# Optimization experiments

Measured on AMD Instinct MI355X. Metric: run time of the kernel, lower is better.

## Reference

```python
import jax, jax.numpy as jnp
import numpy as np
from math import pi

B, CIN, COUT, H, W, K, STRIDE, PAD = 4, 32, 64, 32, 32, 3, 1, 1


def setup_inputs() -> dict:
    key = jax.random.key(0)
    k1, k2, k3 = jax.random.split(key, 3)
    x = jax.random.normal(k1, (B, CIN, H, W), dtype=jnp.float32)
    probe = jax.random.uniform(k2, (1, CIN, COUT, 1, 1, K, K), dtype=jnp.float32, minval=-pi, maxval=pi)
    out_w = jax.random.uniform(k3, (1, CIN, COUT, 1, 1, K, K), dtype=jnp.float32, minval=-pi, maxval=pi)
    return {"x": x, "probe": probe, "out_w": out_w}


def _patches(x):
    # sliding-window gather, equivalent to x.unfold(2,K,S).unfold(3,K,S)
    p = jax.lax.conv_general_dilated_patches(
        x, filter_shape=(K, K), window_strides=(STRIDE, STRIDE),
        padding=[(PAD, PAD), (PAD, PAD)])  # (B, CIN*K*K, Ho, Wo), channel-major
    b, _, ho, wo = p.shape
    p = p.reshape(b, CIN, K, K, ho, wo)
    return jnp.transpose(p, (0, 1, 4, 5, 2, 3))  # (B, CIN, Ho, Wo, K, K)


def reference(x, probe, out_w):
    pat = _patches(x)[:, :, None]                 # (B, CIN, 1, Ho, Wo, K, K)
    act = jnp.cos(pat - probe) ** 3               # (B, CIN, COUT, Ho, Wo, K, K)
    cw = jnp.cos(out_w).reshape(CIN, COUT, K, K)  # squeeze broadcast dims
    sw = jnp.sin(out_w).reshape(CIN, COUT, K, K)
    out_x = jnp.einsum('cokl,bcohwkl->bohw', cw, act)
    out_y = jnp.einsum('cokl,bcohwkl->bohw', sw, act)
    return jnp.arctan2(out_y, out_x)              # (B, COUT, Ho, Wo)
```

## Files before the change

### kernel.cpp

```cpp
#include <hip/hip_runtime.h>
#include <math.h>


typedef _Float16 half8 __attribute__((ext_vector_type(8)));
typedef _Float16 half4 __attribute__((ext_vector_type(4)));
typedef float floatx4 __attribute__((ext_vector_type(4)));

#define B_TAP_STRIDE (16 * 128 * 16)
#define B_VSTRIDE (9u * 16 * 128 * 16)

#define AL_OFF 26112

__global__ __launch_bounds__(256) void ring_prep_b(
    const float* __restrict__ probe, const float* __restrict__ outw,
    char* __restrict__ Bg) {
  int i = blockIdx.x * 256 + threadIdx.x;
  int q = i & 15;
  int n = (i >> 4) & 127;
  int tap = i >> 11;
  int o = n & 63;
  int xy = n >> 6;
  half8 hi, lo;
#pragma unroll
  for (int hf = 0; hf < 2; ++hf) {
    int c = q * 2 + hf;
    int idx = (c * 64 + o) * 9 + tap;
    float th = probe[idx];
    float wvv = outw[idx];
    float sth, cth, sw, cw;
    __sincosf(th, &sth, &cth);
    __sincosf(wvv, &sw, &cw);
    float c3 = cth * fmaf(4.0f * cth, cth, -3.0f);
    float s3 = sth * fmaf(-4.0f * sth, sth, 3.0f);
    float m = xy ? sw : cw;
    float v4[4] = {0.75f * m * cth, 0.75f * m * sth, 0.25f * m * c3,
                   0.25f * m * s3};
#pragma unroll
    for (int f = 0; f < 4; ++f) {
      _Float16 hv = (_Float16)v4[f];
      hi[hf * 4 + f] = hv;
      lo[hf * 4 + f] = (_Float16)((v4[f] - (float)hv) * 2048.0f);
    }
  }
  size_t off = (((size_t)tap * 16 + q) * 128 + n) * 16;
  *(half8*)(Bg + off) = hi;
  *(half8*)(Bg + off + B_VSTRIDE) = lo;
}

#define BLOAD2(dst, base)                    \
  do {                                       \
    dst##0 = *(const half8*)((base));        \
    dst##1 = *(const half8*)((base) + 8192); \
  } while (0)

__global__ __launch_bounds__(512, 2) void ring_mfma(
    const float* __restrict__ x, const char* __restrict__ Bg,
    float* __restrict__ out) {
  __shared__ __align__(16) char sA[52224];
  __shared__ __align__(16) float sR[4096];

  int blk = blockIdx.x;
  int oh = blk & 1;
  int h = (blk >> 1) & 31;
  int b = blk >> 6;
  int tid = threadIdx.x;

  int lane = tid & 63;
  int wv = tid >> 6;
  int n16 = lane & 15;
  int quad = lane >> 4;
  int kg = wv >> 2;
  int xy = (wv >> 1) & 1;
  int og = wv & 1;

  int n_global = xy * 64 + oh * 32 + og * 16 + n16;
  const char* bLane = Bg + (kg * 8 + quad) * 2048 + (size_t)n_global * 16;

  half8 BcH0, BcH1, BcL0, BcL1;
  half8 BnH0, BnH1, BnL0, BnL1;
  half8 BtH0, BtH1, BtL0, BtL1;
  BLOAD2(BcH, bLane);
  BLOAD2(BcL, bLane + B_VSTRIDE);
  BLOAD2(BnH, bLane + B_TAP_STRIDE);
  BLOAD2(BnL, bLane + B_TAP_STRIDE + B_VSTRIDE);

  {
    float xv0[4], xv1[4];
#pragma unroll
    for (int it = 0; it < 4; ++it) {
      int u = tid + it * 512;
      int colidx = u % 34;
      int t = u / 34;
      int q = t & 15;
      int r = t >> 4;
      int hs = h + r - 1;
      int wsx = colidx - 1;
      bool valid = (u < 1632) && ((unsigned)hs < 32u) && ((unsigned)wsx < 32u);
      int xi = ((b * 32 + q * 2) * 32 + ((unsigned)hs < 32u ? hs : 0)) * 32 +
               ((unsigned)wsx < 32u ? wsx : 0);
      xv0[it] = valid ? x[xi] : 0.0f;
      xv1[it] = valid ? x[xi + 1024] : 0.0f;
    }
#pragma unroll
    for (int it = 0; it < 4; ++it) {
      int u = tid + it * 512;
      if (u < 1632) {
        int colidx = u % 34;
        int t = u / 34;
        int q = t & 15;
        int r = t >> 4;
        int p = q ^ (colidx & 7);
        half8 hi, lo;
        float pv2[2] = {xv0[it], xv1[it]};
#pragma unroll
        for (int hf = 0; hf < 2; ++hf) {
          float s1, c1;
          __sincosf(pv2[hf], &s1, &c1);
          float c3 = c1 * fmaf(4.0f * c1, c1, -3.0f);
          float s3 = s1 * fmaf(-4.0f * s1, s1, 3.0f);
          float v4[4] = {c1, s1, c3, s3};
#pragma unroll
          for (int f = 0; f < 4; ++f) {
            _Float16 hv = (_Float16)v4[f];
            hi[hf * 4 + f] = hv;
            lo[hf * 4 + f] = (_Float16)((v4[f] - (float)hv) * 2048.0f);
          }
        }
        int ub = ((r * 34 + colidx) * 16 + p) * 16;
        *(half8*)(sA + ub) = hi;
        *(half8*)(sA + ub + AL_OFF) = lo;
      }
    }
  }

  floatx4 acc0[2], acc1[2], acc2[2];
#pragma unroll
  for (int wt = 0; wt < 2; ++wt) {
    acc0[wt] = (floatx4){0.f, 0.f, 0.f, 0.f};
    acc1[wt] = (floatx4){0.f, 0.f, 0.f, 0.f};
    acc2[wt] = (floatx4){0.f, 0.f, 0.f, 0.f};
  }

  __syncthreads();

#pragma unroll
  for (int tap = 0; tap < 9; ++tap) {
    if (tap < 7) {
      const char* bt = bLane + (size_t)(tap + 2) * B_TAP_STRIDE;
      BLOAD2(BtH, bt);
      BLOAD2(BtL, bt + B_VSTRIDE);
    }

    int dk = tap / 3;
    int l = tap - dk * 3;
#pragma unroll
    for (int wt = 0; wt < 2; ++wt) {
      int colidx = wt * 16 + n16 + l;
      int akey = colidx & 7;
      const char* aH = sA + (dk * 34 + colidx) * 256;
      const char* aL = aH + AL_OFF;
#pragma unroll
      for (int ksl = 0; ksl < 2; ++ksl) {
        int chunk = (kg * 2 + ksl) * 4 + quad;
        int pa = (chunk ^ akey) * 16;
        half8 Ah = *(const half8*)(aH + pa);
        half8 Al = *(const half8*)(aL + pa);
        half8 Bh = ksl ? BcH1 : BcH0;
        half8 Bl = ksl ? BcL1 : BcL0;
        acc0[wt] = __builtin_amdgcn_mfma_f32_16x16x32_f16(Ah, Bh, acc0[wt], 0, 0, 0);
        acc1[wt] = __builtin_amdgcn_mfma_f32_16x16x32_f16(Al, Bh, acc1[wt], 0, 0, 0);
        acc2[wt] = __builtin_amdgcn_mfma_f32_16x16x32_f16(Ah, Bl, acc2[wt], 0, 0, 0);
      }
    }
    BcH0 = BnH0; BcH1 = BnH1; BcL0 = BnL0; BcL1 = BnL1;
    BnH0 = BtH0; BnH1 = BtH1; BnL0 = BtL0; BnL1 = BtL1;
  }

  floatx4 finA = acc0[0] + (acc1[0] + acc2[0]) * (1.0f / 2048.0f);
  floatx4 finB = acc0[1] + (acc1[1] + acc2[1]) * (1.0f / 2048.0f);

  {
    int basei = wv * 512 + n16 * 16 + quad * 4;
    *(floatx4*)(sR + basei) = finA;
    *(floatx4*)(sR + basei + 256) = finB;
  }
  __syncthreads();
  if (tid < 256) {
    int o5 = tid >> 3;
    int wt = (tid >> 2) & 1;
    int q4 = tid & 3;
    int n16r = o5 & 15;
    int ogr = o5 >> 4;
    int sb = wt * 256 + n16r * 16 + q4 * 4;
    floatx4 ax4 = *(const floatx4*)(sR + (0 + ogr) * 512 + sb) +
                  *(const floatx4*)(sR + (4 + ogr) * 512 + sb);
    floatx4 ay4 = *(const floatx4*)(sR + (2 + ogr) * 512 + sb) +
                  *(const floatx4*)(sR + (6 + ogr) * 512 + sb);
    float4 res;
    float* rp = (float*)&res;
#pragma unroll
    for (int r = 0; r < 4; ++r) rp[r] = atan2f(ay4[r], ax4[r]);
    int o = oh * 32 + o5;
    float* dst =
        out + (((size_t)(b * 64 + o) * 32 + h) * 32 + wt * 16 + q4 * 4);
    *(float4*)dst = res;
  }
}

extern "C" void kernel_launch(void* const* d_in, const int* in_sizes, int n_in,
                              void* d_out, int out_size, void* d_ws, size_t ws_size,
                              hipStream_t stream) {
  const float* x = (const float*)d_in[0];
  const float* probe = (const float*)d_in[1];
  const float* outw = (const float*)d_in[2];
  char* Bg = (char*)d_ws;
  float* out = (float*)d_out;

  ring_prep_b<<<72, 256, 0, stream>>>(probe, outw, Bg);
  ring_mfma<<<256, 512, 0, stream>>>(x, Bg, out);
}
```

Baseline: 66.19 us.

## Fuse B-operand preparation into main MFMA kernel via shared-memory probe/weight staging

Removes the separate prep kernel that precomputed split-fp16 B fragments into global workspace. Each block now stages its half of the raw probe and out_w values into shared memory, then computes the trig-based B fragments inside the tap loop just before the MFMAs. This saves a kernel launch and the workspace round trip. In exchange every block redoes the sin/cos work for its weights, and LDS use grows to about 126KB, which may limit occupancy to one block per CU.

```diff
diff --git a/kernel.cpp b/kernel.cpp
--- a/kernel.cpp
+++ b/kernel.cpp
@@ -3,61 +3,19 @@
 
 
 typedef _Float16 half8 __attribute__((ext_vector_type(8)));
-typedef _Float16 half4 __attribute__((ext_vector_type(4)));
 typedef float floatx4 __attribute__((ext_vector_type(4)));
-
-#define B_TAP_STRIDE (16 * 128 * 16)
-#define B_VSTRIDE (9u * 16 * 128 * 16)
+typedef float float2v __attribute__((ext_vector_type(2)));
 
 #define AL_OFF 26112
-
-__global__ __launch_bounds__(256) void ring_prep_b(
-    const float* __restrict__ probe, const float* __restrict__ outw,
-    char* __restrict__ Bg) {
-  int i = blockIdx.x * 256 + threadIdx.x;
-  int q = i & 15;
-  int n = (i >> 4) & 127;
-  int tap = i >> 11;
-  int o = n & 63;
-  int xy = n >> 6;
-  half8 hi, lo;
-#pragma unroll
-  for (int hf = 0; hf < 2; ++hf) {
-    int c = q * 2 + hf;
-    int idx = (c * 64 + o) * 9 + tap;
-    float th = probe[idx];
-    float wvv = outw[idx];
-    float sth, cth, sw, cw;
-    __sincosf(th, &sth, &cth);
-    __sincosf(wvv, &sw, &cw);
-    float c3 = cth * fmaf(4.0f * cth, cth, -3.0f);
-    float s3 = sth * fmaf(-4.0f * sth, sth, 3.0f);
-    float m = xy ? sw : cw;
-    float v4[4] = {0.75f * m * cth, 0.75f * m * sth, 0.25f * m * c3,
-                   0.25f * m * s3};
-#pragma unroll
-    for (int f = 0; f < 4; ++f) {
-      _Float16 hv = (_Float16)v4[f];
-      hi[hf * 4 + f] = hv;
-      lo[hf * 4 + f] = (_Float16)((v4[f] - (float)hv) * 2048.0f);
-    }
-  }
-  size_t off = (((size_t)tap * 16 + q) * 128 + n) * 16;
-  *(half8*)(Bg + off) = hi;
-  *(half8*)(Bg + off + B_VSTRIDE) = lo;
-}
-
-#define BLOAD2(dst, base)                    \
-  do {                                       \
-    dst##0 = *(const half8*)((base));        \
-    dst##1 = *(const half8*)((base) + 8192); \
-  } while (0)
-
-__global__ __launch_bounds__(512, 2) void ring_mfma(
-    const float* __restrict__ x, const char* __restrict__ Bg,
-    float* __restrict__ out) {
-  __shared__ __align__(16) char sA[52224];
-  __shared__ __align__(16) float sR[4096];
+#define SPW_OFF 52224
+
+__global__ __launch_bounds__(512, 2) void ring_one(
+    const float* __restrict__ x, const float* __restrict__ probe,
+    const float* __restrict__ outw, float* __restrict__ out) {
+  __shared__ __align__(16) char sMem[52224 + 73728];
+  char* sA = sMem;
+  float* sPW = (float*)(sMem + SPW_OFF);
+  float* sR = (float*)sMem;
 
   int blk = blockIdx.x;
   int oh = blk & 1;
@@ -73,16 +31,15 @@
   int xy = (wv >> 1) & 1;
   int og = wv & 1;
 
-  int n_global = xy * 64 + oh * 32 + og * 16 + n16;
-  const char* bLane = Bg + (kg * 8 + quad) * 2048 + (size_t)n_global * 16;
-
-  half8 BcH0, BcH1, BcL0, BcL1;
-  half8 BnH0, BnH1, BnL0, BnL1;
-  half8 BtH0, BtH1, BtL0, BtL1;
-  BLOAD2(BcH, bLane);
-  BLOAD2(BcL, bLane + B_VSTRIDE);
-  BLOAD2(BnH, bLane + B_TAP_STRIDE);
-  BLOAD2(BnL, bLane + B_TAP_STRIDE + B_VSTRIDE);
+#pragma unroll
+  for (int it = 0; it < 18; ++it) {
+    int j = tid + it * 512;
+    int c = j / 288;
+    int rem = j - c * 288;
+    int g = c * 576 + oh * 288 + rem;
+    float2v pw = {probe[g], outw[g]};
+    *(float2v*)(sPW + 2 * j) = pw;
+  }
 
   {
     float xv0[4], xv1[4];
@@ -133,6 +90,12 @@
     }
   }
 
+  int ol = og * 16 + n16;
+  int jb0 = ((kg * 8 + quad) * 2 + 0) * 288 + ol * 9;
+  int jb1 = ((kg * 8 + quad) * 2 + 1) * 288 + ol * 9;
+  int jb2 = ((kg * 8 + quad + 4) * 2 + 0) * 288 + ol * 9;
+  int jb3 = ((kg * 8 + quad + 4) * 2 + 1) * 288 + ol * 9;
+
   floatx4 acc0[2], acc1[2], acc2[2];
 #pragma unroll
   for (int wt = 0; wt < 2; ++wt) {
@@ -145,10 +108,33 @@
 
 #pragma unroll
   for (int tap = 0; tap < 9; ++tap) {
-    if (tap < 7) {
-      const char* bt = bLane + (size_t)(tap + 2) * B_TAP_STRIDE;
-      BLOAD2(BtH, bt);
-      BLOAD2(BtL, bt + B_VSTRIDE);
+    half8 BH0, BH1, BL0, BL1;
+#pragma unroll
+    for (int e = 0; e < 4; ++e) {
+      int jb = (e == 0) ? jb0 : (e == 1) ? jb1 : (e == 2) ? jb2 : jb3;
+      float2v pw = *(const float2v*)(sPW + 2 * (jb + tap));
+      float th = pw[0];
+      float wvv = pw[1];
+      float sth, cth;
+      __sincosf(th, &sth, &cth);
+      float m = xy ? __sinf(wvv) : __cosf(wvv);
+      float c3 = cth * fmaf(4.0f * cth, cth, -3.0f);
+      float s3 = sth * fmaf(-4.0f * sth, sth, 3.0f);
+      float m75 = 0.75f * m, m25 = 0.25f * m;
+      float v4[4] = {m75 * cth, m75 * sth, m25 * c3, m25 * s3};
+      int ehf = e & 1;
+#pragma unroll
+      for (int f = 0; f < 4; ++f) {
+        _Float16 hv = (_Float16)v4[f];
+        _Float16 lv = (_Float16)((v4[f] - (float)hv) * 2048.0f);
+        if (e < 2) {
+          BH0[ehf * 4 + f] = hv;
+          BL0[ehf * 4 + f] = lv;
+        } else {
+          BH1[ehf * 4 + f] = hv;
+          BL1[ehf * 4 + f] = lv;
+        }
+      }
     }
 
     int dk = tap / 3;
@@ -165,20 +151,19 @@
         int pa = (chunk ^ akey) * 16;
         half8 Ah = *(const half8*)(aH + pa);
         half8 Al = *(const half8*)(aL + pa);
-        half8 Bh = ksl ? BcH1 : BcH0;
-        half8 Bl = ksl ? BcL1 : BcL0;
+        half8 Bh = ksl ? BH1 : BH0;
+        half8 Bl = ksl ? BL1 : BL0;
         acc0[wt] = __builtin_amdgcn_mfma_f32_16x16x32_f16(Ah, Bh, acc0[wt], 0, 0, 0);
         acc1[wt] = __builtin_amdgcn_mfma_f32_16x16x32_f16(Al, Bh, acc1[wt], 0, 0, 0);
         acc2[wt] = __builtin_amdgcn_mfma_f32_16x16x32_f16(Ah, Bl, acc2[wt], 0, 0, 0);
       }
     }
-    BcH0 = BnH0; BcH1 = BnH1; BcL0 = BnL0; BcL1 = BnL1;
-    BnH0 = BtH0; BnH1 = BtH1; BnL0 = BtL0; BnL1 = BtL1;
   }
 
   floatx4 finA = acc0[0] + (acc1[0] + acc2[0]) * (1.0f / 2048.0f);
   floatx4 finB = acc0[1] + (acc1[1] + acc2[1]) * (1.0f / 2048.0f);
 
+  __syncthreads();
   {
     int basei = wv * 512 + n16 * 16 + quad * 4;
     *(floatx4*)(sR + basei) = finA;
@@ -213,9 +198,9 @@
   const float* x = (const float*)d_in[0];
   const float* probe = (const float*)d_in[1];
   const float* outw = (const float*)d_in[2];
-  char* Bg = (char*)d_ws;
   float* out = (float*)d_out;
-
-  ring_prep_b<<<72, 256, 0, stream>>>(probe, outw, Bg);
-  ring_mfma<<<256, 512, 0, stream>>>(x, Bg, out);
+  (void)d_ws;
+  (void)ws_size;
+
+  ring_one<<<256, 512, 0, stream>>>(x, probe, outw, out);
 }
```

Result: no change. 66.79 us (+0.9%).

## Split width tiles across waves using 1024-thread blocks in ring_mfma

Applied to the files above, without the earlier changes.

Doubles the block size to 1024 threads so that each wave handles a single 16-column width tile instead of two. This halves the per-wave MFMA and accumulator work and cuts B prefetching from two taps ahead to one. The epilogue now has every thread compute one scalar atan2 and store it, replacing the float4 path that used only half the threads. The gain is more waves per block and lower register pressure per wave. The costs are that every wave loads the same B fragments twice, the prefetch distance is shorter, and the output stores are scalar.

```diff
diff --git a/kernel.cpp b/kernel.cpp
--- a/kernel.cpp
+++ b/kernel.cpp
@@ -3,7 +3,6 @@
 
 
 typedef _Float16 half8 __attribute__((ext_vector_type(8)));
-typedef _Float16 half4 __attribute__((ext_vector_type(4)));
 typedef float floatx4 __attribute__((ext_vector_type(4)));
 
 #define B_TAP_STRIDE (16 * 128 * 16)
@@ -53,7 +52,7 @@
     dst##1 = *(const half8*)((base) + 8192); \
   } while (0)
 
-__global__ __launch_bounds__(512, 2) void ring_mfma(
+__global__ __launch_bounds__(1024) void ring_mfma(
     const float* __restrict__ x, const char* __restrict__ Bg,
     float* __restrict__ out) {
   __shared__ __align__(16) char sA[52224];
@@ -69,26 +68,24 @@
   int wv = tid >> 6;
   int n16 = lane & 15;
   int quad = lane >> 4;
-  int kg = wv >> 2;
+  int og = wv & 1;
   int xy = (wv >> 1) & 1;
-  int og = wv & 1;
+  int kg = (wv >> 2) & 1;
+  int wt = wv >> 3;
 
   int n_global = xy * 64 + oh * 32 + og * 16 + n16;
   const char* bLane = Bg + (kg * 8 + quad) * 2048 + (size_t)n_global * 16;
 
   half8 BcH0, BcH1, BcL0, BcL1;
   half8 BnH0, BnH1, BnL0, BnL1;
-  half8 BtH0, BtH1, BtL0, BtL1;
   BLOAD2(BcH, bLane);
   BLOAD2(BcL, bLane + B_VSTRIDE);
-  BLOAD2(BnH, bLane + B_TAP_STRIDE);
-  BLOAD2(BnL, bLane + B_TAP_STRIDE + B_VSTRIDE);
 
   {
-    float xv0[4], xv1[4];
-#pragma unroll
-    for (int it = 0; it < 4; ++it) {
-      int u = tid + it * 512;
+    float xv0[2], xv1[2];
+#pragma unroll
+    for (int it = 0; it < 2; ++it) {
+      int u = tid + it * 1024;
       int colidx = u % 34;
       int t = u / 34;
       int q = t & 15;
@@ -102,8 +99,8 @@
       xv1[it] = valid ? x[xi + 1024] : 0.0f;
     }
 #pragma unroll
-    for (int it = 0; it < 4; ++it) {
-      int u = tid + it * 512;
+    for (int it = 0; it < 2; ++it) {
+      int u = tid + it * 1024;
       if (u < 1632) {
         int colidx = u % 34;
         int t = u / 34;
@@ -133,77 +130,62 @@
     }
   }
 
-  floatx4 acc0[2], acc1[2], acc2[2];
-#pragma unroll
-  for (int wt = 0; wt < 2; ++wt) {
-    acc0[wt] = (floatx4){0.f, 0.f, 0.f, 0.f};
-    acc1[wt] = (floatx4){0.f, 0.f, 0.f, 0.f};
-    acc2[wt] = (floatx4){0.f, 0.f, 0.f, 0.f};
-  }
+  floatx4 acc0 = {0.f, 0.f, 0.f, 0.f};
+  floatx4 acc1 = {0.f, 0.f, 0.f, 0.f};
+  floatx4 acc2 = {0.f, 0.f, 0.f, 0.f};
 
   __syncthreads();
 
 #pragma unroll
   for (int tap = 0; tap < 9; ++tap) {
-    if (tap < 7) {
-      const char* bt = bLane + (size_t)(tap + 2) * B_TAP_STRIDE;
-      BLOAD2(BtH, bt);
-      BLOAD2(BtL, bt + B_VSTRIDE);
+    if (tap < 8) {
+      const char* bt = bLane + (size_t)(tap + 1) * B_TAP_STRIDE;
+      BLOAD2(BnH, bt);
+      BLOAD2(BnL, bt + B_VSTRIDE);
     }
 
     int dk = tap / 3;
     int l = tap - dk * 3;
-#pragma unroll
-    for (int wt = 0; wt < 2; ++wt) {
-      int colidx = wt * 16 + n16 + l;
-      int akey = colidx & 7;
-      const char* aH = sA + (dk * 34 + colidx) * 256;
-      const char* aL = aH + AL_OFF;
-#pragma unroll
-      for (int ksl = 0; ksl < 2; ++ksl) {
-        int chunk = (kg * 2 + ksl) * 4 + quad;
-        int pa = (chunk ^ akey) * 16;
-        half8 Ah = *(const half8*)(aH + pa);
-        half8 Al = *(const half8*)(aL + pa);
-        half8 Bh = ksl ? BcH1 : BcH0;
-        half8 Bl = ksl ? BcL1 : BcL0;
-        acc0[wt] = __builtin_amdgcn_mfma_f32_16x16x32_f16(Ah, Bh, acc0[wt], 0, 0, 0);
-        acc1[wt] = __builtin_amdgcn_mfma_f32_16x16x32_f16(Al, Bh, acc1[wt], 0, 0, 0);
-        acc2[wt] = __builtin_amdgcn_mfma_f32_16x16x32_f16(Ah, Bl, acc2[wt], 0, 0, 0);
-      }
+    int colidx = wt * 16 + n16 + l;
+    int akey = colidx & 7;
+    const char* aH = sA + (dk * 34 + colidx) * 256;
+    const char* aL = aH + AL_OFF;
+#pragma unroll
+    for (int ksl = 0; ksl < 2; ++ksl) {
+      int chunk = (kg * 2 + ksl) * 4 + quad;
+      int pa = (chunk ^ akey) * 16;
+      half8 Ah = *(const half8*)(aH + pa);
+      half8 Al = *(const half8*)(aL + pa);
+      half8 Bh = ksl ? BcH1 : BcH0;
+      half8 Bl = ksl ? BcL1 : BcL0;
+      acc0 = __builtin_amdgcn_mfma_f32_16x16x32_f16(Ah, Bh, acc0, 0, 0, 0);
+      acc1 = __builtin_amdgcn_mfma_f32_16x16x32_f16(Al, Bh, acc1, 0, 0, 0);
+      acc2 = __builtin_amdgcn_mfma_f32_16x16x32_f16(Ah, Bl, acc2, 0, 0, 0);
     }
     BcH0 = BnH0; BcH1 = BnH1; BcL0 = BnL0; BcL1 = BnL1;
-    BnH0 = BtH0; BnH1 = BtH1; BnL0 = BtL0; BnL1 = BtL1;
-  }
-
-  floatx4 finA = acc0[0] + (acc1[0] + acc2[0]) * (1.0f / 2048.0f);
-  floatx4 finB = acc0[1] + (acc1[1] + acc2[1]) * (1.0f / 2048.0f);
+  }
+
+  floatx4 fin = acc0 + (acc1 + acc2) * (1.0f / 2048.0f);
 
   {
-    int basei = wv * 512 + n16 * 16 + quad * 4;
-    *(floatx4*)(sR + basei) = finA;
-    *(floatx4*)(sR + basei + 256) = finB;
+    int basei = wv * 256 + n16 * 16 + quad * 4;
+    *(floatx4*)(sR + basei) = fin;
   }
   __syncthreads();
-  if (tid < 256) {
-    int o5 = tid >> 3;
-    int wt = (tid >> 2) & 1;
-    int q4 = tid & 3;
+  {
+    int o5 = tid >> 5;
+    int w5 = tid & 31;
+    int ogr = o5 >> 4;
     int n16r = o5 & 15;
-    int ogr = o5 >> 4;
-    int sb = wt * 256 + n16r * 16 + q4 * 4;
-    floatx4 ax4 = *(const floatx4*)(sR + (0 + ogr) * 512 + sb) +
-                  *(const floatx4*)(sR + (4 + ogr) * 512 + sb);
-    floatx4 ay4 = *(const floatx4*)(sR + (2 + ogr) * 512 + sb) +
-                  *(const floatx4*)(sR + (6 + ogr) * 512 + sb);
-    float4 res;
-    float* rp = (float*)&res;
-#pragma unroll
-    for (int r = 0; r < 4; ++r) rp[r] = atan2f(ay4[r], ax4[r]);
-    int o = oh * 32 + o5;
-    float* dst =
-        out + (((size_t)(b * 64 + o) * 32 + h) * 32 + wt * 16 + q4 * 4);
-    *(float4*)dst = res;
+    int wtr = w5 >> 4;
+    int mr = w5 & 15;
+    int sb = n16r * 16 + mr;
+    float ax = sR[(wtr * 8 + 0 + ogr) * 256 + sb] +
+               sR[(wtr * 8 + 4 + ogr) * 256 + sb];
+    float ay = sR[(wtr * 8 + 2 + ogr) * 256 + sb] +
+               sR[(wtr * 8 + 6 + ogr) * 256 + sb];
+    float res = atan2f(ay, ax);
+    out[(((size_t)(b * 64 + oh * 32 + o5) * 32 + h) * 32) + w5] = res;
   }
 }
 
@@ -217,5 +199,5 @@
   float* out = (float*)d_out;
 
   ring_prep_b<<<72, 256, 0, stream>>>(probe, outw, Bg);
-  ring_mfma<<<256, 512, 0, stream>>>(x, Bg, out);
+  ring_mfma<<<256, 1024, 0, stream>>>(x, Bg, out);
 }
```

Measured after the change: 66.73 us. Within noise of the previous version (+0.8%).
